# Kernel optimization log

Measured on AMD Instinct MI355X. Metric: run time of the kernel, lower is better.

The kernel has to match this reference:

```python
import jax, jax.numpy as jnp
import numpy as np
from jax import lax

LAYERS = 4
B, C, D1, D2, D3, D4 = 2, 3, 48, 48, 48, 24

_DN = lax.ConvDimensionNumbers(lhs_spec=(0, 1, 2, 3, 4, 5),
                               rhs_spec=(0, 1, 2, 3, 4, 5),
                               out_spec=(0, 1, 2, 3, 4, 5))


def conv4d(x, w, b, pad):
    # x: (B, Cin, D1, D2, D3, D4); w: (Cout, Cin, k1, k2, k3, k4); pad: 4-tuple
    y = lax.conv_general_dilated(x, w, window_strides=(1, 1, 1, 1),
                                 padding=[(p, p) for p in pad],
                                 dimension_numbers=_DN)
    return y + b.reshape(1, -1, 1, 1, 1, 1)


def setup_inputs() -> dict:
    key = jax.random.key(0)
    ks = jax.random.split(key, 10)
    s = 0.05
    return {
        "f": jax.random.normal(ks[0], (B, C, D1, D2, D3, D4), jnp.float32),
        "bondary": jax.random.normal(ks[1], (B, C, D1, D2, D3, D4), jnp.float32),
        "Wg": jax.random.normal(ks[2], (LAYERS, 3, 6, 3, 3, 3, 3), jnp.float32) * s,
        "bg": jax.random.normal(ks[3], (LAYERS, 3), jnp.float32) * s,
        "W1": jax.random.normal(ks[4], (LAYERS, 3, 3, 3, 3, 3, 1), jnp.float32) * s,
        "b1": jax.random.normal(ks[5], (LAYERS, 3), jnp.float32) * s,
        "W2": jax.random.normal(ks[6], (LAYERS, 3, 3, 1, 1, 1, 3), jnp.float32) * s,
        "b2": jax.random.normal(ks[7], (LAYERS, 3), jnp.float32) * s,
        "Wd": jax.random.normal(ks[8], (LAYERS, 3, 3, 1, 1, 1, 1), jnp.float32) * s,
        "bd": jax.random.normal(ks[9], (LAYERS, 3), jnp.float32) * s,
    }


def reference(f, bondary, Wg, bg, W1, b1, W2, b2, Wd, bd):
    out = f
    for i in range(LAYERS):
        temp = jnp.concatenate((out, bondary), axis=1)          # (B, 6, ...)
        temp = conv4d(temp, Wg[i], bg[i], (1, 1, 1, 1))          # gather
        temp = conv4d(temp, W1[i], b1[i], (1, 1, 1, 0))          # (3,3,3,1)
        out = conv4d(temp, W2[i], b2[i], (0, 0, 0, 1)) \
            + conv4d(out, Wd[i], bd[i], (0, 0, 0, 0))            # residual
    return out
```

## Files before the change

### kernel.cpp

```cpp
#include <hip/hip_runtime.h>

typedef _Float16 half2_t __attribute__((ext_vector_type(2)));

#if __has_builtin(__builtin_amdgcn_fdot2)
#define FDOT2(a, b, c) __builtin_amdgcn_fdot2((a), (b), (c), false)
#else
__device__ __forceinline__ float FDOT2(half2_t a, half2_t b, float c) {
    return c + (float)a.x * (float)b.x + (float)a.y * (float)b.y;
}
#endif

namespace {
constexpr int D  = 48;
constexpr int D4 = 24;
constexpr int S2 = D * D4;
constexpr int S1 = D * S2;
constexpr int SC = D * S1;
constexpr int NB = 2;
constexpr int NELEM = NB * 3 * SC;
constexpr int NPAIR_H2 = NB * 3 * SC;
}


__global__ __launch_bounds__(256) void pack_weights(
        const float* __restrict__ Wg, half2_t* __restrict__ pw)
{
    int i = blockIdx.x * 256 + threadIdx.x;
    const int NTOT = 4 * 3 * 27 * 9;
    if (i >= NTOT) return;
    int k4 = i % 3; int r = i / 3;
    int co = r % 3; r /= 3;
    int k123 = r % 27; r /= 27;
    int p = r % 3; int l = r / 3;
    int ciA = 2 * p, ciB = 2 * p + 1;
    float a = Wg[((l * 3 + co) * 6 + ciA) * 81 + k123 * 3 + k4];
    float b = Wg[((l * 3 + co) * 6 + ciB) * 81 + k123 * 3 + k4];
    pw[i] = half2_t{(_Float16)a, (_Float16)b};
}

__global__ __launch_bounds__(256) void pack_init(
        const float* __restrict__ f, const float* __restrict__ bnd,
        half2_t* __restrict__ pairs)
{
    int i = blockIdx.x * 256 + threadIdx.x;
    int plane = i / (SC / 4);
    int zz = (i % (SC / 4)) * 4;
    int b = plane / 3, p = plane % 3;
    const float* A; const float* Bc;
    if (p == 0)      { A = f   + (size_t)(b*3 + 0) * SC; Bc = f   + (size_t)(b*3 + 1) * SC; }
    else if (p == 1) { A = f   + (size_t)(b*3 + 2) * SC; Bc = bnd + (size_t)(b*3 + 0) * SC; }
    else             { A = bnd + (size_t)(b*3 + 1) * SC; Bc = bnd + (size_t)(b*3 + 2) * SC; }
    float4 a = *(const float4*)(A + zz);
    float4 c = *(const float4*)(Bc + zz);
    union { float4 f4; half2_t h[4]; } u;
    u.h[0] = half2_t{(_Float16)a.x, (_Float16)c.x};
    u.h[1] = half2_t{(_Float16)a.y, (_Float16)c.y};
    u.h[2] = half2_t{(_Float16)a.z, (_Float16)c.z};
    u.h[3] = half2_t{(_Float16)a.w, (_Float16)c.w};
    *(float4*)(pairs + (size_t)plane * SC + zz) = u.f4;
}

__global__ __launch_bounds__(256) void convA(
        const half2_t* __restrict__ pairs, const half2_t* __restrict__ pw,
        const float* __restrict__ bg, _Float16* __restrict__ dst)
{
    int t = blockIdx.x * 256 + threadIdx.x;
    int x3 = t % D; int r = t / D;
    int x2 = r % D; r /= D;
    int x1 = r % D; int b = r / D;

    float acc[3][D4];
#pragma unroll
    for (int c = 0; c < 3; ++c) {
        float bb = bg[c];
#pragma unroll
        for (int j = 0; j < D4; ++j) acc[c][j] = bb;
    }

#pragma unroll 1
    for (int p = 0; p < 3; ++p) {
        const half2_t* src = pairs + (size_t)(b*3 + p) * SC;
#pragma unroll 1
        for (int k1 = 0; k1 < 3; ++k1) {
            int z1 = x1 + k1 - 1;
            if ((unsigned)z1 >= (unsigned)D) continue;
            const half2_t* src1 = src + z1 * S1;
#pragma unroll
            for (int k2 = 0; k2 < 3; ++k2) {
                int z2 = x2 + k2 - 1;
                if ((unsigned)z2 >= (unsigned)D) continue;
#pragma unroll
                for (int k3 = 0; k3 < 3; ++k3) {
                    int z3 = x3 + k3 - 1;
                    if ((unsigned)z3 >= (unsigned)D) continue;
                    half2_t v[26];
                    v[0] = half2_t{0, 0}; v[25] = half2_t{0, 0};
                    const float4* L = (const float4*)(src1 + z2 * S2 + z3 * D4);
#pragma unroll
                    for (int q = 0; q < 6; ++q) {
                        union { float4 f4; half2_t h[4]; } u;
                        u.f4 = L[q];
                        v[1 + 4*q + 0] = u.h[0];
                        v[1 + 4*q + 1] = u.h[1];
                        v[1 + 4*q + 2] = u.h[2];
                        v[1 + 4*q + 3] = u.h[3];
                    }
                    const half2_t* w = pw + (size_t)((p * 27 + (k1*9 + k2*3 + k3)) * 9);
#pragma unroll
                    for (int co = 0; co < 3; ++co) {
                        half2_t w0 = w[co*3 + 0];
                        half2_t w1 = w[co*3 + 1];
                        half2_t w2 = w[co*3 + 2];
#pragma unroll
                        for (int j = 0; j < D4; ++j) {
                            float a = acc[co][j];
                            a = FDOT2(w0, v[j],     a);
                            a = FDOT2(w1, v[j + 1], a);
                            a = FDOT2(w2, v[j + 2], a);
                            acc[co][j] = a;
                        }
                    }
                }
            }
        }
    }

    int spos = x1 * S1 + x2 * S2 + x3 * D4;
#pragma unroll
    for (int co = 0; co < 3; ++co) {
        union { float4 f4[3]; _Float16 h[24]; } u;
#pragma unroll
        for (int j = 0; j < D4; ++j) u.h[j] = (_Float16)acc[co][j];
        float4* o4 = (float4*)(dst + (b*3 + co) * (size_t)SC + spos);
#pragma unroll
        for (int q = 0; q < 3; ++q) o4[q] = u.f4[q];
    }
}

__global__ __launch_bounds__(256) void convBC(
        const _Float16* __restrict__ t1, half2_t* pairs,
        const float* __restrict__ W1, const float* __restrict__ b1,
        const float* __restrict__ W2, const float* __restrict__ b2,
        const float* __restrict__ Wd, const float* __restrict__ bd,
        float* __restrict__ dstF32, int writeF32)
{
    int t = blockIdx.x * 256 + threadIdx.x;
    int x3 = t % D; int r = t / D;
    int x2 = r % D; r /= D;
    int x1 = r % D; int b = r / D;

    int spos = x1 * S1 + x2 * S2 + x3 * D4;

    float t2[3][D4];
#pragma unroll
    for (int c = 0; c < 3; ++c) {
        float bb = b1[c];
#pragma unroll
        for (int j = 0; j < D4; ++j) t2[c][j] = bb;
    }

#pragma unroll 1
    for (int ci = 0; ci < 3; ++ci) {
        const _Float16* src = t1 + (b*3 + ci) * (size_t)SC;
#pragma unroll 1
        for (int k1 = 0; k1 < 3; ++k1) {
            int z1 = x1 + k1 - 1;
            if ((unsigned)z1 >= (unsigned)D) continue;
            const _Float16* src1 = src + z1 * S1;
#pragma unroll
            for (int k2 = 0; k2 < 3; ++k2) {
                int z2 = x2 + k2 - 1;
                if ((unsigned)z2 >= (unsigned)D) continue;
#pragma unroll
                for (int k3 = 0; k3 < 3; ++k3) {
                    int z3 = x3 + k3 - 1;
                    if ((unsigned)z3 >= (unsigned)D) continue;
                    const float4* L = (const float4*)(src1 + z2 * S2 + z3 * D4);
                    float v[D4];
#pragma unroll
                    for (int q = 0; q < 3; ++q) {
                        union { float4 f4; half2_t h[4]; } u;
                        u.f4 = L[q];
#pragma unroll
                        for (int m = 0; m < 4; ++m) {
                            v[8*q + 2*m + 0] = (float)u.h[m].x;
                            v[8*q + 2*m + 1] = (float)u.h[m].y;
                        }
                    }
                    int kk = k1*9 + k2*3 + k3;
                    float wA = W1[  0 + ci*27 + kk];
                    float wB = W1[ 81 + ci*27 + kk];
                    float wC = W1[162 + ci*27 + kk];
#pragma unroll
                    for (int j = 0; j < D4; ++j) {
                        t2[0][j] += wA * v[j];
                        t2[1][j] += wB * v[j];
                        t2[2][j] += wC * v[j];
                    }
                }
            }
        }
    }

    half2_t* p0ptr = pairs + (size_t)(b*3 + 0) * SC + spos;
    half2_t* p1ptr = pairs + (size_t)(b*3 + 1) * SC + spos;
    half2_t rp0[D4], rp1[D4];
#pragma unroll
    for (int q = 0; q < 6; ++q) {
        union { float4 f4; half2_t h[4]; } u;
        u.f4 = ((const float4*)p0ptr)[q];
        rp0[4*q+0]=u.h[0]; rp0[4*q+1]=u.h[1]; rp0[4*q+2]=u.h[2]; rp0[4*q+3]=u.h[3];
        u.f4 = ((const float4*)p1ptr)[q];
        rp1[4*q+0]=u.h[0]; rp1[4*q+1]=u.h[1]; rp1[4*q+2]=u.h[2]; rp1[4*q+3]=u.h[3];
    }

    float U[3][3][3];
#pragma unroll
    for (int co = 0; co < 3; ++co)
#pragma unroll
        for (int ci = 0; ci < 3; ++ci)
#pragma unroll
            for (int k = 0; k < 3; ++k)
                U[co][ci][k] = W2[co*9 + ci*3 + k];
    float WD[9];
#pragma unroll
    for (int i = 0; i < 9; ++i) WD[i] = Wd[i];
    float c0 = b2[0] + bd[0], c1 = b2[1] + bd[1], c2 = b2[2] + bd[2];

    float o0[D4], o1[D4], o2[D4];
#pragma unroll
    for (int j = 0; j < D4; ++j) {
        float s0 = c0, s1 = c1, s2 = c2;
#pragma unroll
        for (int ci = 0; ci < 3; ++ci) {
            float tm = (j > 0)  ? t2[ci][j-1] : 0.f;
            float tc = t2[ci][j];
            float tp = (j < 23) ? t2[ci][j+1] : 0.f;
            s0 += U[0][ci][0]*tm + U[0][ci][1]*tc + U[0][ci][2]*tp;
            s1 += U[1][ci][0]*tm + U[1][ci][1]*tc + U[1][ci][2]*tp;
            s2 += U[2][ci][0]*tm + U[2][ci][1]*tc + U[2][ci][2]*tp;
        }
        float pv0 = (float)rp0[j].x, pv1 = (float)rp0[j].y, pv2 = (float)rp1[j].x;
        s0 += WD[0]*pv0 + WD[1]*pv1 + WD[2]*pv2;
        s1 += WD[3]*pv0 + WD[4]*pv1 + WD[5]*pv2;
        s2 += WD[6]*pv0 + WD[7]*pv1 + WD[8]*pv2;
        o0[j] = s0; o1[j] = s1; o2[j] = s2;
    }

    {
        union { float4 f4[6]; half2_t h[24]; } u0, u1;
#pragma unroll
        for (int j = 0; j < D4; ++j) {
            u0.h[j] = half2_t{(_Float16)o0[j], (_Float16)o1[j]};
            u1.h[j] = half2_t{(_Float16)o2[j], rp1[j].y};
        }
#pragma unroll
        for (int q = 0; q < 6; ++q) {
            ((float4*)p0ptr)[q] = u0.f4[q];
            ((float4*)p1ptr)[q] = u1.f4[q];
        }
    }

    if (writeF32) {
        float* d0 = dstF32 + (size_t)(b*3 + 0) * SC + spos;
        float* d1 = dstF32 + (size_t)(b*3 + 1) * SC + spos;
        float* d2 = dstF32 + (size_t)(b*3 + 2) * SC + spos;
#pragma unroll
        for (int q = 0; q < 6; ++q) {
            ((float4*)d0)[q] = make_float4(o0[4*q], o0[4*q+1], o0[4*q+2], o0[4*q+3]);
            ((float4*)d1)[q] = make_float4(o1[4*q], o1[4*q+1], o1[4*q+2], o1[4*q+3]);
            ((float4*)d2)[q] = make_float4(o2[4*q], o2[4*q+1], o2[4*q+2], o2[4*q+3]);
        }
    }
}

extern "C" void kernel_launch(void* const* d_in, const int* in_sizes, int n_in,
                              void* d_out, int out_size, void* d_ws, size_t ws_size,
                              hipStream_t stream)
{
    const float* f   = (const float*)d_in[0];
    const float* bnd = (const float*)d_in[1];
    const float* Wg  = (const float*)d_in[2];
    const float* bg  = (const float*)d_in[3];
    const float* W1  = (const float*)d_in[4];
    const float* b1  = (const float*)d_in[5];
    const float* W2  = (const float*)d_in[6];
    const float* b2  = (const float*)d_in[7];
    const float* Wd  = (const float*)d_in[8];
    const float* bd  = (const float*)d_in[9];

    _Float16* t1h   = (_Float16*)d_ws;
    half2_t*  pairs = (half2_t*)(t1h + NELEM);
    half2_t*  pw    = pairs + NPAIR_H2;

    pack_weights<<<dim3((2916 + 255) / 256), dim3(256), 0, stream>>>(Wg, pw);
    pack_init<<<dim3(NB * 3 * (SC / 4) / 256), dim3(256), 0, stream>>>(f, bnd, pairs);

    const int grid = NB * D * D * D / 256;
    for (int l = 0; l < 4; ++l) {
        convA<<<dim3(grid), dim3(256), 0, stream>>>(pairs, pw + l * 729, bg + l*3, t1h);
        convBC<<<dim3(grid), dim3(256), 0, stream>>>(
            t1h, pairs, W1 + l*243, b1 + l*3, W2 + l*27, b2 + l*3,
            Wd + l*9, bd + l*3, (float*)d_out, l == 3 ? 1 : 0);
    }
}
```

Before: 1.067 ms.

## Split each thread's D4 row into two halves to double thread count

Each thread of convA and convBC now computes 12 of the 24 innermost outputs, with a halo window loaded around its half, and the grid is doubled accordingly. The goal is fewer accumulator registers per thread, which allows higher occupancy and more parallelism. In exchange, overlapping halo loads are issued redundantly and W1 taps are recomputed for halo elements in convBC. Warps stay uniform because the half index is chosen per block range.

```diff
diff --git a/kernel.cpp b/kernel.cpp
--- a/kernel.cpp
+++ b/kernel.cpp
@@ -19,6 +19,7 @@
 constexpr int NB = 2;
 constexpr int NELEM = NB * 3 * SC;
 constexpr int NPAIR_H2 = NB * 3 * SC;
+constexpr int NS = NB * D * D * D;
 }
 
 
@@ -60,21 +61,30 @@
     *(float4*)(pairs + (size_t)plane * SC + zz) = u.f4;
 }
 
-__global__ __launch_bounds__(256) void convA(
-        const half2_t* __restrict__ pairs, const half2_t* __restrict__ pw,
+
+struct VWin { union { float4 f4[4]; half2_t h[16]; } u; };
+
+template<int H>
+__device__ __forceinline__ half2_t hv(const VWin& V, int i)
+{
+    return (i < 0 || i > 15) ? half2_t{(_Float16)0, (_Float16)0} : V.u.h[i];
+}
+
+template<int H>
+__device__ __forceinline__ void convA_body(
+        int s, const half2_t* __restrict__ pairs, const half2_t* __restrict__ pw,
         const float* __restrict__ bg, _Float16* __restrict__ dst)
 {
-    int t = blockIdx.x * 256 + threadIdx.x;
-    int x3 = t % D; int r = t / D;
+    int x3 = s % D; int r = s / D;
     int x2 = r % D; r /= D;
     int x1 = r % D; int b = r / D;
 
-    float acc[3][D4];
+    float acc[3][12];
 #pragma unroll
     for (int c = 0; c < 3; ++c) {
         float bb = bg[c];
 #pragma unroll
-        for (int j = 0; j < D4; ++j) acc[c][j] = bb;
+        for (int j = 0; j < 12; ++j) acc[c][j] = bb;
     }
 
 #pragma unroll 1
@@ -93,18 +103,10 @@
                 for (int k3 = 0; k3 < 3; ++k3) {
                     int z3 = x3 + k3 - 1;
                     if ((unsigned)z3 >= (unsigned)D) continue;
-                    half2_t v[26];
-                    v[0] = half2_t{0, 0}; v[25] = half2_t{0, 0};
-                    const float4* L = (const float4*)(src1 + z2 * S2 + z3 * D4);
-#pragma unroll
-                    for (int q = 0; q < 6; ++q) {
-                        union { float4 f4; half2_t h[4]; } u;
-                        u.f4 = L[q];
-                        v[1 + 4*q + 0] = u.h[0];
-                        v[1 + 4*q + 1] = u.h[1];
-                        v[1 + 4*q + 2] = u.h[2];
-                        v[1 + 4*q + 3] = u.h[3];
-                    }
+                    VWin V;
+                    const float4* L = (const float4*)(src1 + z2 * S2 + z3 * D4 + 8*H);
+#pragma unroll
+                    for (int q = 0; q < 4; ++q) V.u.f4[q] = L[q];
                     const half2_t* w = pw + (size_t)((p * 27 + (k1*9 + k2*3 + k3)) * 9);
 #pragma unroll
                     for (int co = 0; co < 3; ++co) {
@@ -112,11 +114,11 @@
                         half2_t w1 = w[co*3 + 1];
                         half2_t w2 = w[co*3 + 2];
 #pragma unroll
-                        for (int j = 0; j < D4; ++j) {
+                        for (int j = 0; j < 12; ++j) {
                             float a = acc[co][j];
-                            a = FDOT2(w0, v[j],     a);
-                            a = FDOT2(w1, v[j + 1], a);
-                            a = FDOT2(w2, v[j + 2], a);
+                            a = FDOT2(w0, hv<H>(V, 4*H + j - 1), a);
+                            a = FDOT2(w1, hv<H>(V, 4*H + j    ), a);
+                            a = FDOT2(w2, hv<H>(V, 4*H + j + 1), a);
                             acc[co][j] = a;
                         }
                     }
@@ -125,38 +127,52 @@
         }
     }
 
-    int spos = x1 * S1 + x2 * S2 + x3 * D4;
+    int spos = x1 * S1 + x2 * S2 + x3 * D4 + 12*H;
 #pragma unroll
     for (int co = 0; co < 3; ++co) {
-        union { float4 f4[3]; _Float16 h[24]; } u;
-#pragma unroll
-        for (int j = 0; j < D4; ++j) u.h[j] = (_Float16)acc[co][j];
-        float4* o4 = (float4*)(dst + (b*3 + co) * (size_t)SC + spos);
-#pragma unroll
-        for (int q = 0; q < 3; ++q) o4[q] = u.f4[q];
-    }
-}
-
-__global__ __launch_bounds__(256) void convBC(
-        const _Float16* __restrict__ t1, half2_t* pairs,
+        union { float2 f2[3]; _Float16 h[12]; } u;
+#pragma unroll
+        for (int j = 0; j < 12; ++j) u.h[j] = (_Float16)acc[co][j];
+        float2* o2 = (float2*)(dst + (b*3 + co) * (size_t)SC + spos);
+#pragma unroll
+        for (int q = 0; q < 3; ++q) o2[q] = u.f2[q];
+    }
+}
+
+__global__ __launch_bounds__(256) void convA(
+        const half2_t* __restrict__ pairs, const half2_t* __restrict__ pw,
+        const float* __restrict__ bg, _Float16* __restrict__ dst)
+{
+    int t = blockIdx.x * 256 + threadIdx.x;
+    if (t < NS) convA_body<0>(t, pairs, pw, bg, dst);
+    else        convA_body<1>(t - NS, pairs, pw, bg, dst);
+}
+
+
+template<int H>
+__device__ __forceinline__ void convBC_body(
+        int s, const _Float16* __restrict__ t1, half2_t* pairs,
         const float* __restrict__ W1, const float* __restrict__ b1,
         const float* __restrict__ W2, const float* __restrict__ b2,
         const float* __restrict__ Wd, const float* __restrict__ bd,
         float* __restrict__ dstF32, int writeF32)
 {
-    int t = blockIdx.x * 256 + threadIdx.x;
-    int x3 = t % D; int r = t / D;
+    int x3 = s % D; int r = s / D;
     int x2 = r % D; r /= D;
     int x1 = r % D; int b = r / D;
 
     int spos = x1 * S1 + x2 * S2 + x3 * D4;
 
-    float t2[3][D4];
+    constexpr int M0 = (H == 0) ? 1 : 0;
+    constexpr int M1 = (H == 0) ? 13 : 12;
+
+    float t2l[3][14];
 #pragma unroll
     for (int c = 0; c < 3; ++c) {
         float bb = b1[c];
 #pragma unroll
-        for (int j = 0; j < D4; ++j) t2[c][j] = bb;
+        for (int m = 0; m < 14; ++m)
+            t2l[c][m] = (m >= M0 && m <= M1) ? bb : 0.f;
     }
 
 #pragma unroll 1
@@ -175,38 +191,33 @@
                 for (int k3 = 0; k3 < 3; ++k3) {
                     int z3 = x3 + k3 - 1;
                     if ((unsigned)z3 >= (unsigned)D) continue;
-                    const float4* L = (const float4*)(src1 + z2 * S2 + z3 * D4);
-                    float v[D4];
-#pragma unroll
-                    for (int q = 0; q < 3; ++q) {
-                        union { float4 f4; half2_t h[4]; } u;
-                        u.f4 = L[q];
-#pragma unroll
-                        for (int m = 0; m < 4; ++m) {
-                            v[8*q + 2*m + 0] = (float)u.h[m].x;
-                            v[8*q + 2*m + 1] = (float)u.h[m].y;
-                        }
-                    }
+                    const float4* L = (const float4*)(src1 + z2 * S2 + z3 * D4 + 8*H);
+                    union { float4 f4[2]; half2_t h[8]; } u;
+                    u.f4[0] = L[0];
+                    u.f4[1] = L[1];
                     int kk = k1*9 + k2*3 + k3;
                     float wA = W1[  0 + ci*27 + kk];
                     float wB = W1[ 81 + ci*27 + kk];
                     float wC = W1[162 + ci*27 + kk];
 #pragma unroll
-                    for (int j = 0; j < D4; ++j) {
-                        t2[0][j] += wA * v[j];
-                        t2[1][j] += wB * v[j];
-                        t2[2][j] += wC * v[j];
+                    for (int m = M0; m <= M1; ++m) {
+                        int li = 4*H + m - 1;
+                        half2_t hh = u.h[li >> 1];
+                        float v = (li & 1) ? (float)hh.y : (float)hh.x;
+                        t2l[0][m] += wA * v;
+                        t2l[1][m] += wB * v;
+                        t2l[2][m] += wC * v;
                     }
                 }
             }
         }
     }
 
-    half2_t* p0ptr = pairs + (size_t)(b*3 + 0) * SC + spos;
-    half2_t* p1ptr = pairs + (size_t)(b*3 + 1) * SC + spos;
-    half2_t rp0[D4], rp1[D4];
-#pragma unroll
-    for (int q = 0; q < 6; ++q) {
+    half2_t* p0ptr = pairs + (size_t)(b*3 + 0) * SC + spos + 12*H;
+    half2_t* p1ptr = pairs + (size_t)(b*3 + 1) * SC + spos + 12*H;
+    half2_t rp0[12], rp1[12];
+#pragma unroll
+    for (int q = 0; q < 3; ++q) {
         union { float4 f4; half2_t h[4]; } u;
         u.f4 = ((const float4*)p0ptr)[q];
         rp0[4*q+0]=u.h[0]; rp0[4*q+1]=u.h[1]; rp0[4*q+2]=u.h[2]; rp0[4*q+3]=u.h[3];
@@ -227,51 +238,63 @@
     for (int i = 0; i < 9; ++i) WD[i] = Wd[i];
     float c0 = b2[0] + bd[0], c1 = b2[1] + bd[1], c2 = b2[2] + bd[2];
 
-    float o0[D4], o1[D4], o2[D4];
-#pragma unroll
-    for (int j = 0; j < D4; ++j) {
+    float o0[12], o1[12], o2[12];
+#pragma unroll
+    for (int n = 0; n < 12; ++n) {
         float s0 = c0, s1 = c1, s2 = c2;
 #pragma unroll
         for (int ci = 0; ci < 3; ++ci) {
-            float tm = (j > 0)  ? t2[ci][j-1] : 0.f;
-            float tc = t2[ci][j];
-            float tp = (j < 23) ? t2[ci][j+1] : 0.f;
+            float tm = t2l[ci][n + 0];
+            float tc = t2l[ci][n + 1];
+            float tp = t2l[ci][n + 2];
             s0 += U[0][ci][0]*tm + U[0][ci][1]*tc + U[0][ci][2]*tp;
             s1 += U[1][ci][0]*tm + U[1][ci][1]*tc + U[1][ci][2]*tp;
             s2 += U[2][ci][0]*tm + U[2][ci][1]*tc + U[2][ci][2]*tp;
         }
-        float pv0 = (float)rp0[j].x, pv1 = (float)rp0[j].y, pv2 = (float)rp1[j].x;
+        float pv0 = (float)rp0[n].x, pv1 = (float)rp0[n].y, pv2 = (float)rp1[n].x;
         s0 += WD[0]*pv0 + WD[1]*pv1 + WD[2]*pv2;
         s1 += WD[3]*pv0 + WD[4]*pv1 + WD[5]*pv2;
         s2 += WD[6]*pv0 + WD[7]*pv1 + WD[8]*pv2;
-        o0[j] = s0; o1[j] = s1; o2[j] = s2;
+        o0[n] = s0; o1[n] = s1; o2[n] = s2;
     }
 
     {
-        union { float4 f4[6]; half2_t h[24]; } u0, u1;
-#pragma unroll
-        for (int j = 0; j < D4; ++j) {
-            u0.h[j] = half2_t{(_Float16)o0[j], (_Float16)o1[j]};
-            u1.h[j] = half2_t{(_Float16)o2[j], rp1[j].y};
-        }
-#pragma unroll
-        for (int q = 0; q < 6; ++q) {
+        union { float4 f4[3]; half2_t h[12]; } u0, u1;
+#pragma unroll
+        for (int n = 0; n < 12; ++n) {
+            u0.h[n] = half2_t{(_Float16)o0[n], (_Float16)o1[n]};
+            u1.h[n] = half2_t{(_Float16)o2[n], rp1[n].y};
+        }
+#pragma unroll
+        for (int q = 0; q < 3; ++q) {
             ((float4*)p0ptr)[q] = u0.f4[q];
             ((float4*)p1ptr)[q] = u1.f4[q];
         }
     }
 
     if (writeF32) {
-        float* d0 = dstF32 + (size_t)(b*3 + 0) * SC + spos;
-        float* d1 = dstF32 + (size_t)(b*3 + 1) * SC + spos;
-        float* d2 = dstF32 + (size_t)(b*3 + 2) * SC + spos;
-#pragma unroll
-        for (int q = 0; q < 6; ++q) {
+        float* d0 = dstF32 + (size_t)(b*3 + 0) * SC + spos + 12*H;
+        float* d1 = dstF32 + (size_t)(b*3 + 1) * SC + spos + 12*H;
+        float* d2 = dstF32 + (size_t)(b*3 + 2) * SC + spos + 12*H;
+#pragma unroll
+        for (int q = 0; q < 3; ++q) {
             ((float4*)d0)[q] = make_float4(o0[4*q], o0[4*q+1], o0[4*q+2], o0[4*q+3]);
             ((float4*)d1)[q] = make_float4(o1[4*q], o1[4*q+1], o1[4*q+2], o1[4*q+3]);
             ((float4*)d2)[q] = make_float4(o2[4*q], o2[4*q+1], o2[4*q+2], o2[4*q+3]);
         }
     }
+}
+
+__global__ __launch_bounds__(256) void convBC(
+        const _Float16* __restrict__ t1, half2_t* pairs,
+        const float* __restrict__ W1, const float* __restrict__ b1,
+        const float* __restrict__ W2, const float* __restrict__ b2,
+        const float* __restrict__ Wd, const float* __restrict__ bd,
+        float* __restrict__ dstF32, int writeF32)
+{
+    int t = blockIdx.x * 256 + threadIdx.x;
+    if (t < NS) convBC_body<0>(t, t1, pairs, W1, b1, W2, b2, Wd, bd, dstF32, writeF32);
+    else        convBC_body<1>(t - NS, t1, pairs, W1, b1, W2, b2, Wd, bd, dstF32, writeF32);
 }
 
 extern "C" void kernel_launch(void* const* d_in, const int* in_sizes, int n_in,
@@ -296,7 +319,7 @@
     pack_weights<<<dim3((2916 + 255) / 256), dim3(256), 0, stream>>>(Wg, pw);
     pack_init<<<dim3(NB * 3 * (SC / 4) / 256), dim3(256), 0, stream>>>(f, bnd, pairs);
 
-    const int grid = NB * D * D * D / 256;
+    const int grid = 2 * NS / 256;
     for (int l = 0; l < 4; ++l) {
         convA<<<dim3(grid), dim3(256), 0, stream>>>(pairs, pw + l * 729, bg + l*3, t1h);
         convBC<<<dim3(grid), dim3(256), 0, stream>>>(
```

Result: slower. 1.361 ms (+27.6%).
